# Kernel optimization log

Measured on AMD Instinct MI355X. Metric: run time of the kernel, lower is better.

## Reference

```python
import jax, jax.numpy as jnp
import numpy as np

B, N, F, Tf, Tm, Df, Dm = 8, 128, 128, 64, 256, 32, 128
E, H, TE = 64, 128, 64  # node_emb_dim, hidden_dim, time_emb_dim


def setup_inputs() -> dict:
    key = jax.random.key(0)
    ks = jax.random.split(key, 16)
    s = 0.05
    return {
        'noisy_adj': jax.random.normal(ks[0], (B, N, N), jnp.float32),
        'node_feats': jax.random.normal(ks[1], (B, N, F), jnp.float32),
        'feat_fnirs': jax.random.normal(ks[2], (B, N, Tf, Df), jnp.float32),
        'feat_music': jax.random.normal(ks[3], (B, 1, Tm, Dm), jnp.float32),
        'g_pre': jax.random.normal(ks[4], (B, N, N), jnp.float32),
        'node_W': jax.random.normal(ks[5], (F, E), jnp.float32) * s,
        'node_b': jnp.zeros((E,), jnp.float32),
        'fnirs_W': jax.random.normal(ks[6], (Df, H), jnp.float32) * s,
        'fnirs_b': jnp.zeros((H,), jnp.float32),
        'music_W': jax.random.normal(ks[7], (Dm, H), jnp.float32) * s,
        'music_b': jnp.zeros((H,), jnp.float32),
        'mlp_W1': jax.random.normal(ks[8], (2 * E + 2 + H + TE, H), jnp.float32) * s,
        'mlp_b1': jnp.zeros((H,), jnp.float32),
        'mlp_W2': jax.random.normal(ks[9], (H, 1), jnp.float32) * s,
        'mlp_b2': jnp.zeros((1,), jnp.float32),
        't': jax.random.randint(ks[10], (B,), 0, Tf),
    }


def _time_embedding(t_idx):
    # sinusoidal timestep embedding -> [B, TE]
    half = TE // 2
    inv_freq = jnp.exp(-jnp.arange(half, dtype=jnp.float32) * (jnp.log(10000.0) / (half - 1)))
    freqs = t_idx.astype(jnp.float32)[:, None] * inv_freq  # [B, half]
    return jnp.concatenate([jnp.sin(freqs), jnp.cos(freqs)], axis=-1)


def _conditional(feat_fnirs, feat_music, fnirs_W, fnirs_b, music_W, music_b):
    # cross-attention: fNIRS timesteps attend over music timesteps
    q = feat_fnirs @ fnirs_W + fnirs_b          # [B,N,Tf,H]
    kv = feat_music @ music_W + music_b         # [B,1,Tm,H]
    scale = 1.0 / jnp.sqrt(jnp.float32(H))
    scores = jnp.einsum('bnfh,bomh->bnfm', q, kv) * scale  # [B,N,Tf,Tm]
    attn = jax.nn.softmax(scores, axis=-1)
    ctx = jnp.einsum('bnfm,bomh->bnfh', attn, kv)
    fused = q + ctx                              # [B,N,Tf,H]
    attn_weights = attn.mean(axis=1)             # mean across channels -> [B,Tf,Tm]
    ent = -(attn * jnp.log(attn + 1e-8)).sum(-1)
    attention_loss = ent.mean()
    return fused, attn_weights, attention_loss


def reference(noisy_adj, node_feats, feat_fnirs, feat_music, g_pre,
              node_W, node_b, fnirs_W, fnirs_b, music_W, music_b,
              mlp_W1, mlp_b1, mlp_W2, mlp_b2, t):
    h = node_feats @ node_W + node_b             # [B,N,E]

    fused, attn_weights, attention_loss = _conditional(
        feat_fnirs, feat_music, fnirs_W, fnirs_b, music_W, music_b)

    t_idx = jnp.clip(t, 0, fused.shape[2] - 1)
    # gather conditional state at diffusion step t -> [B,N,H]
    idx = jnp.broadcast_to(t_idx[:, None, None, None], (B, N, 1, H))
    cond_t = jnp.take_along_axis(fused, idx, axis=2)[:, :, 0, :]

    time_emb = _time_embedding(t_idx)            # [B,TE]

    # Fused edge MLP layer-1: split W1 along the concat axis instead of
    # materializing the [B,N,N,in_dim] concat tensor (same math).
    W1_hi = mlp_W1[:E]
    W1_hj = mlp_W1[E:2 * E]
    w_adj = mlp_W1[2 * E]          # [H]
    w_gpre = mlp_W1[2 * E + 1]     # [H]
    W1_cond = mlp_W1[2 * E + 2:2 * E + 2 + H]
    W1_time = mlp_W1[2 * E + 2 + H:]

    pre = ((h @ W1_hi)[:, :, None, :]            # h_i varies over row i
           + (h @ W1_hj)[:, None, :, :]          # h_j varies over col j
           + noisy_adj[..., None] * w_adj
           + g_pre[..., None] * w_gpre
           + (cond_t @ W1_cond)[:, None, :, :]   # cond broadcast over row i
           + (time_emb @ W1_time)[:, None, None, :]
           + mlp_b1)                             # [B,N,N,H]
    hid = jax.nn.relu(pre)
    noise_pred = (hid @ mlp_W2)[..., 0] + mlp_b2[0]  # [B,N,N]
    return noise_pred, attn_weights, attention_loss
```

## Files before the change

kernel.cpp:

```cpp
#include <hip/hip_runtime.h>
#include <hip/hip_bf16.h>

#define Bn  8
#define Nn  128
#define Fn  128
#define Tfn 64
#define Tmn 256
#define Dfn 32
#define Dmn 128
#define En  64
#define Hn  128
#define TEn 64

#define OUT_AW_OFF   (Bn*Nn*Nn)
#define OUT_LOSS_OFF (Bn*Nn*Nn + Bn*Tfn*Tmn)

#define WS_G     0
#define WS_BIAS  32768
#define WS_KVT   34816
#define WS_FWT   165888
#define WS_NWT   167936
#define WS_HIT   172032
#define WS_HJT   176128
#define WS_CONDT 180224
#define WS_TVEC  188416
#define WS_PI    189440
#define WS_PJ    320512
#define WS_LOSS  451584

#define SCALE 0.08838834764831845f

typedef __attribute__((ext_vector_type(8))) short short8;
typedef __attribute__((ext_vector_type(4))) float f32x4;

__device__ __forceinline__ unsigned short f2bf(float x) {
  __hip_bfloat16 h = __float2bfloat16(x);
  return __builtin_bit_cast(unsigned short, h);
}
__device__ __forceinline__ unsigned int pk2(float a, float b) {
  return (unsigned int)f2bf(a) | ((unsigned int)f2bf(b) << 16);
}

__global__ __launch_bounds__(128) void k_prep(
    const float* __restrict__ feat_music, const float* __restrict__ music_W,
    const float* __restrict__ music_b, const float* __restrict__ fnirs_W,
    const float* __restrict__ fnirs_b,
    const float* __restrict__ W1, const float* __restrict__ b1,
    const float* __restrict__ node_W, const int* __restrict__ t,
    unsigned short* __restrict__ kvT, unsigned short* __restrict__ G_bf,
    float* __restrict__ bias,
    unsigned short* __restrict__ fwt, unsigned short* __restrict__ nwt,
    unsigned short* __restrict__ hit, unsigned short* __restrict__ hjt,
    unsigned short* __restrict__ condt, float* __restrict__ tvec,
    float* __restrict__ loss_acc)
{
  __shared__ float fm_s[Dmn];
  __shared__ float kv_s[Hn];
  __shared__ float red[2];
  __shared__ float te_l[TEn];
  int tid = threadIdx.x;

  if (blockIdx.x < 2048) {
    int b = blockIdx.x >> 8;
    int m = blockIdx.x & 255;
    fm_s[tid] = feat_music[((size_t)b*Tmn + m)*Dmn + tid];
    __syncthreads();
    float a = music_b[tid];
    #pragma unroll 8
    for (int d = 0; d < Dmn; d++) a = fmaf(fm_s[d], music_W[d*Hn + tid], a);
    kv_s[tid] = a;
    kvT[((size_t)b*Hn + tid)*Tmn + m] = f2bf(a);
    float bp = fnirs_b[tid] * a;
    bp += __shfl_xor(bp, 32); bp += __shfl_xor(bp, 16); bp += __shfl_xor(bp, 8);
    bp += __shfl_xor(bp, 4);  bp += __shfl_xor(bp, 2);  bp += __shfl_xor(bp, 1);
    if ((tid & 63) == 0) red[tid >> 6] = bp;
    __syncthreads();
    int d = tid >> 2, qd = tid & 3;
    float g = 0.f;
    #pragma unroll 8
    for (int hh = 0; hh < 32; hh++) {
      int h = hh*4 + qd;
      g = fmaf(fnirs_W[d*Hn + h], kv_s[h], g);
    }
    g += __shfl_xor(g, 1); g += __shfl_xor(g, 2);
    if (qd == 0) G_bf[((size_t)b*Tmn + m)*Dfn + d] = f2bf(g * SCALE);
    if (tid == 0) bias[b*Tmn + m] = (red[0] + red[1]) * SCALE;
    return;
  }

  int blk = blockIdx.x - 2048;
  if (blk < 8) {
    int b = blk;
    if (tid < TEn/2) {
      int tcl = min(max(t[b], 0), Tfn - 1);
      float fr = (float)tcl * __expf(-(float)tid * (logf(10000.f) / (TEn/2 - 1)));
      te_l[tid] = __sinf(fr);
      te_l[tid + TEn/2] = __cosf(fr);
    }
    __syncthreads();
    float a = b1[tid];
    #pragma unroll 8
    for (int u = 0; u < TEn; u++) a = fmaf(te_l[u], W1[(2*En + 2 + Hn + u)*Hn + tid], a);
    tvec[b*Hn + tid] = a;
    if (b == 0 && tid == 0) loss_acc[0] = 0.f;
  } else if (blk < 16) {
    int q = blk - 8;
    #pragma unroll 4
    for (int i = 0; i < 16; i++) {
      int k = q*16 + i;
      condt[k*Hn + tid] = f2bf(W1[(2*En + 2 + tid)*Hn + k]);
    }
  } else if (blk < 20) {
    int q = blk - 16;
    int e = tid & 63, kh = tid >> 6;
    #pragma unroll 4
    for (int i = 0; i < 16; i++) {
      int k = q*32 + kh*16 + i;
      hit[k*En + e] = f2bf(W1[e*Hn + k]);
    }
  } else if (blk < 24) {
    int q = blk - 20;
    int e = tid & 63, kh = tid >> 6;
    #pragma unroll 4
    for (int i = 0; i < 16; i++) {
      int k = q*32 + kh*16 + i;
      hjt[k*En + e] = f2bf(W1[(En + e)*Hn + k]);
    }
  } else if (blk < 32) {
    int q = blk - 24;
    int fl = tid & 15, eh = tid >> 4;
    #pragma unroll 4
    for (int i = 0; i < 8; i++) {
      int e = eh*8 + i;
      nwt[e*Fn + q*16 + fl] = f2bf(node_W[(q*16 + fl)*En + e]);
    }
  } else if (blk < 34) {
    int q = blk - 32;
    int d = tid & 31, hh = tid >> 5;
    #pragma unroll 4
    for (int i = 0; i < 16; i++) {
      int h = q*64 + hh*16 + i;
      fwt[h*Dfn + d] = f2bf(fnirs_W[d*Hn + h]);
    }
  }
}

struct SmemAttn {
  unsigned short feat_l[Nn][40];
  unsigned short G_l[Tmn][40];
  float bias_l[Tmn];
  float aw_l[4][Tmn];
  float ent_l[4];
};
struct SmemCond {
  unsigned short featT_l[16][40];
  unsigned short A_l[16][264];
  unsigned short nf_l[16][136];
  unsigned short h_l[16][72];
  unsigned short cond_l[16][136];
  float sS[4][16];
  float tvec_l[Hn];
};
union __align__(16) SmemK2 {
  SmemAttn a;
  SmemCond c;
};

__global__ __launch_bounds__(256, 2) void k_attn_cond(
    const float* __restrict__ feat_fnirs, const float* __restrict__ node_feats,
    const float* __restrict__ node_b, const int* __restrict__ t,
    const unsigned short* __restrict__ G_bf, const float* __restrict__ bias,
    const unsigned short* __restrict__ kvT, const unsigned short* __restrict__ fwt,
    const unsigned short* __restrict__ nwt, const unsigned short* __restrict__ hit,
    const unsigned short* __restrict__ hjt, const unsigned short* __restrict__ condt,
    const float* __restrict__ tvec, float* __restrict__ Pi, float* __restrict__ Pj,
    float* __restrict__ aw_out, float* __restrict__ loss_acc)
{
  __shared__ SmemK2 smem;
  int tid = threadIdx.x;
  int lane = tid & 63, wv = tid >> 6;
  int col = lane & 15, kq = lane >> 4;

  if (blockIdx.x < 512) {
    int b = blockIdx.x >> 6, f = blockIdx.x & 63;
    {
      const uint4* gg = (const uint4*)(G_bf + (size_t)b*Tmn*Dfn);
      #pragma unroll
      for (int v0 = 0; v0 < 4; v0++) {
        int v = tid + v0*256;
        uint4 x = gg[v];
        int m = v >> 2, qt = v & 3;
        *((uint4*)&smem.a.G_l[m][qt*8]) = x;
      }
      smem.a.bias_l[tid] = bias[b*Tmn + tid];
      int n = tid >> 1, hf = tid & 1;
      const float* src = feat_fnirs + (((size_t)b*Nn + n)*Tfn + f)*Dfn + hf*16;
      float4 x0 = ((const float4*)src)[0];
      float4 x1 = ((const float4*)src)[1];
      float4 x2 = ((const float4*)src)[2];
      float4 x3 = ((const float4*)src)[3];
      uint4 pa, pb;
      pa.x = pk2(x0.x, x0.y); pa.y = pk2(x0.z, x0.w);
      pa.z = pk2(x1.x, x1.y); pa.w = pk2(x1.z, x1.w);
      pb.x = pk2(x2.x, x2.y); pb.y = pk2(x2.z, x2.w);
      pb.z = pk2(x3.x, x3.y); pb.w = pk2(x3.z, x3.w);
      uint4* dst = (uint4*)&smem.a.feat_l[n][hf*16];
      dst[0] = pa; dst[1] = pb;
    }
    __syncthreads();

    int n0 = wv * 32;
    short8 a0 = *(const short8*)&smem.a.feat_l[n0 + col][kq*8];
    short8 a1 = *(const short8*)&smem.a.feat_l[n0 + 16 + col][kq*8];

    float S0[4] = {0,0,0,0}, S1[4] = {0,0,0,0};
    float T0[4] = {0,0,0,0}, T1[4] = {0,0,0,0};
    float p0[16][4], p1[16][4];

    #pragma unroll
    for (int mt = 0; mt < 16; mt++) {
      short8 bfr = *(const short8*)&smem.a.G_l[mt*16 + col][kq*8];
      float bv = smem.a.bias_l[mt*16 + col];
      f32x4 c0 = __builtin_amdgcn_mfma_f32_16x16x32_bf16(a0, bfr, (f32x4){0.f,0.f,0.f,0.f}, 0, 0, 0);
      f32x4 c1 = __builtin_amdgcn_mfma_f32_16x16x32_bf16(a1, bfr, (f32x4){0.f,0.f,0.f,0.f}, 0, 0, 0);
      #pragma unroll
      for (int r = 0; r < 4; r++) {
        float sc = c0[r] + bv;
        float p = __expf(sc);
        S0[r] += p; T0[r] = fmaf(p, sc, T0[r]); p0[mt][r] = p;
        sc = c1[r] + bv;
        p = __expf(sc);
        S1[r] += p; T1[r] = fmaf(p, sc, T1[r]); p1[mt][r] = p;
      }
    }

    #pragma unroll
    for (int r = 0; r < 4; r++) {
      #pragma unroll
      for (int off = 1; off < 16; off <<= 1) {
        S0[r] += __shfl_xor(S0[r], off);
        S1[r] += __shfl_xor(S1[r], off);
        T0[r] += __shfl_xor(T0[r], off);
        T1[r] += __shfl_xor(T1[r], off);
      }
    }
    float i0v[4], i1v[4];
    #pragma unroll
    for (int r = 0; r < 4; r++) { i0v[r] = 1.f / S0[r]; i1v[r] = 1.f / S1[r]; }

    float ent = 0.f;
    if (col == 0) {
      #pragma unroll
      for (int r = 0; r < 4; r++) {
        ent += (__logf(S0[r]) - T0[r] * i0v[r]);
        ent += (__logf(S1[r]) - T1[r] * i1v[r]);
      }
    }
    ent += __shfl_xor(ent, 32); ent += __shfl_xor(ent, 16);
    ent += __shfl_xor(ent, 8);  ent += __shfl_xor(ent, 4);
    ent += __shfl_xor(ent, 2);  ent += __shfl_xor(ent, 1);
    if (lane == 0) smem.a.ent_l[wv] = ent;

    #pragma unroll
    for (int mt = 0; mt < 16; mt++) {
      float a = 0.f;
      #pragma unroll
      for (int r = 0; r < 4; r++) {
        a = fmaf(p0[mt][r], i0v[r], a);
        a = fmaf(p1[mt][r], i1v[r], a);
      }
      a += __shfl_xor(a, 16);
      a += __shfl_xor(a, 32);
      if (lane < 16) smem.a.aw_l[wv][mt*16 + lane] = a;
    }
    __syncthreads();

    float s = (smem.a.aw_l[0][tid] + smem.a.aw_l[1][tid]) +
              (smem.a.aw_l[2][tid] + smem.a.aw_l[3][tid]);
    aw_out[((size_t)b*Tfn + f)*Tmn + tid] = s * (1.f/(float)Nn);
    if (tid == 0)
      atomicAdd(loss_acc, (smem.a.ent_l[0] + smem.a.ent_l[1]) +
                          (smem.a.ent_l[2] + smem.a.ent_l[3]));
    return;
  }

  int blk = blockIdx.x - 512;
  int b = blk >> 3;
  int i0 = (blk & 7) << 4;
  int tcl = min(max(t[b], 0), Tfn - 1);

  if (tid < 128) {
    int i = tid >> 3, c = (tid & 7) * 4;
    const float* src = feat_fnirs + (((size_t)b*Nn + i0 + i)*Tfn + tcl)*Dfn + c;
    float4 x = *(const float4*)src;
    *(unsigned int*)&smem.c.featT_l[i][c]     = pk2(x.x, x.y);
    *(unsigned int*)&smem.c.featT_l[i][c + 2] = pk2(x.z, x.w);
    smem.c.tvec_l[tid] = tvec[b*Hn + tid];
  }
  {
    int i = tid >> 4, c = (tid & 15) * 8;
    const float* src = node_feats + ((size_t)b*Nn + i0 + i)*Fn + c;
    float4 x0 = ((const float4*)src)[0];
    float4 x1 = ((const float4*)src)[1];
    *(unsigned int*)&smem.c.nf_l[i][c]     = pk2(x0.x, x0.y);
    *(unsigned int*)&smem.c.nf_l[i][c + 2] = pk2(x0.z, x0.w);
    *(unsigned int*)&smem.c.nf_l[i][c + 4] = pk2(x1.x, x1.y);
    *(unsigned int*)&smem.c.nf_l[i][c + 6] = pk2(x1.z, x1.w);
  }
  __syncthreads();

  short8 a_feat = *(const short8*)&smem.c.featT_l[col][kq*8];

  float p[4][4];
  float Sp[4] = {0,0,0,0};
  #pragma unroll
  for (int mtl = 0; mtl < 4; mtl++) {
    int mt = wv*4 + mtl;
    short8 bg = *(const short8*)(G_bf + ((size_t)b*Tmn + mt*16 + col)*Dfn + kq*8);
    f32x4 c = __builtin_amdgcn_mfma_f32_16x16x32_bf16(a_feat, bg, (f32x4){0.f,0.f,0.f,0.f}, 0, 0, 0);
    float bv = bias[b*Tmn + mt*16 + col];
    #pragma unroll
    for (int r = 0; r < 4; r++) {
      float pp = __expf(c[r] + bv);
      p[mtl][r] = pp;
      Sp[r] += pp;
    }
  }
  #pragma unroll
  for (int r = 0; r < 4; r++) {
    float v = Sp[r];
    v += __shfl_xor(v, 1); v += __shfl_xor(v, 2);
    v += __shfl_xor(v, 4); v += __shfl_xor(v, 8);
    Sp[r] = v;
  }
  if (col == 0) {
    #pragma unroll
    for (int r = 0; r < 4; r++) smem.c.sS[wv][kq*4 + r] = Sp[r];
  }
  __syncthreads();
  float invS[4];
  #pragma unroll
  for (int r = 0; r < 4; r++)
    invS[r] = 1.f / (smem.c.sS[0][kq*4+r] + smem.c.sS[1][kq*4+r] +
                     smem.c.sS[2][kq*4+r] + smem.c.sS[3][kq*4+r]);
  #pragma unroll
  for (int mtl = 0; mtl < 4; mtl++) {
    #pragma unroll
    for (int r = 0; r < 4; r++)
      smem.c.A_l[kq*4 + r][(wv*4 + mtl)*16 + col] = f2bf(p[mtl][r] * invS[r]);
  }
  __syncthreads();

  f32x4 accC0 = {0.f,0.f,0.f,0.f}, accC1 = {0.f,0.f,0.f,0.f};
  {
    int ct0 = wv*2, ct1 = wv*2 + 1;
    short8 bq0 = *(const short8*)(fwt + (size_t)(ct0*16 + col)*Dfn + kq*8);
    short8 bq1 = *(const short8*)(fwt + (size_t)(ct1*16 + col)*Dfn + kq*8);
    accC0 = __builtin_amdgcn_mfma_f32_16x16x32_bf16(a_feat, bq0, accC0, 0, 0, 0);
    accC1 = __builtin_amdgcn_mfma_f32_16x16x32_bf16(a_feat, bq1, accC1, 0, 0, 0);
    #pragma unroll
    for (int ks = 0; ks < 8; ks++) {
      short8 aA = *(const short8*)&smem.c.A_l[col][ks*32 + kq*8];
      short8 bk0 = *(const short8*)(kvT + ((size_t)b*Hn + ct0*16 + col)*Tmn + ks*32 + kq*8);
      short8 bk1 = *(const short8*)(kvT + ((size_t)b*Hn + ct1*16 + col)*Tmn + ks*32 + kq*8);
      accC0 = __builtin_amdgcn_mfma_f32_16x16x32_bf16(aA, bk0, accC0, 0, 0, 0);
      accC1 = __builtin_amdgcn_mfma_f32_16x16x32_bf16(aA, bk1, accC1, 0, 0, 0);
    }
  }
  f32x4 accH = {0.f,0.f,0.f,0.f};
  #pragma unroll
  for (int ks = 0; ks < 4; ks++) {
    short8 aN = *(const short8*)&smem.c.nf_l[col][ks*32 + kq*8];
    short8 bn = *(const short8*)(nwt + (size_t)(wv*16 + col)*Fn + ks*32 + kq*8);
    accH = __builtin_amdgcn_mfma_f32_16x16x32_bf16(aN, bn, accH, 0, 0, 0);
  }
  float nb = node_b[wv*16 + col];
  #pragma unroll
  for (int r = 0; r < 4; r++) {
    smem.c.cond_l[kq*4 + r][(wv*2    )*16 + col] = f2bf(accC0[r]);
    smem.c.cond_l[kq*4 + r][(wv*2 + 1)*16 + col] = f2bf(accC1[r]);
    smem.c.h_l[kq*4 + r][wv*16 + col] = f2bf(accH[r] + nb);
  }
  __syncthreads();

  short8 aH[2];
  aH[0] = *(const short8*)&smem.c.h_l[col][kq*8];
  aH[1] = *(const short8*)&smem.c.h_l[col][32 + kq*8];
  #pragma unroll
  for (int ctl = 0; ctl < 2; ctl++) {
    int ct = wv*2 + ctl;
    f32x4 accPi = {0.f,0.f,0.f,0.f}, accPj = {0.f,0.f,0.f,0.f};
    #pragma unroll
    for (int ks = 0; ks < 2; ks++) {
      short8 bi_ = *(const short8*)(hit + (size_t)(ct*16 + col)*En + ks*32 + kq*8);
      short8 bj_ = *(const short8*)(hjt + (size_t)(ct*16 + col)*En + ks*32 + kq*8);
      accPi = __builtin_amdgcn_mfma_f32_16x16x32_bf16(aH[ks], bi_, accPi, 0, 0, 0);
      accPj = __builtin_amdgcn_mfma_f32_16x16x32_bf16(aH[ks], bj_, accPj, 0, 0, 0);
    }
    #pragma unroll
    for (int ks = 0; ks < 4; ks++) {
      short8 aC = *(const short8*)&smem.c.cond_l[col][ks*32 + kq*8];
      short8 bc = *(const short8*)(condt + (size_t)(ct*16 + col)*Hn + ks*32 + kq*8);
      accPj = __builtin_amdgcn_mfma_f32_16x16x32_bf16(aC, bc, accPj, 0, 0, 0);
    }
    float tv = smem.c.tvec_l[ct*16 + col];
    #pragma unroll
    for (int r = 0; r < 4; r++) {
      size_t row = (size_t)b*Nn + i0 + kq*4 + r;
      Pi[row*Hn + ct*16 + col] = accPi[r];
      Pj[row*Hn + ct*16 + col] = accPj[r] + tv;
    }
  }
}

__global__ __launch_bounds__(256) void k_edge(
    const float* __restrict__ adj, const float* __restrict__ gpre,
    const float* __restrict__ W1, const float* __restrict__ W2,
    const float* __restrict__ b2p, const float* __restrict__ Pi,
    const float* __restrict__ Pj, float* __restrict__ out,
    const float* __restrict__ loss_acc)
{
  int b  = blockIdx.x >> 6;
  int ib = (blockIdx.x >> 1) & 31;
  int jh = blockIdx.x & 1;
  int i0 = ib * 4;
  int tid = threadIdx.x;

  __shared__ float4 Pj_s4[64*32];
  __shared__ float4 Pi_s4[4*32];
  __shared__ float4 w2_s[32], wa_s[32], wg_s[32];

  {
    const float4* Pjg = (const float4*)(Pj + ((size_t)b*Nn + jh*64)*Hn);
    #pragma unroll
    for (int v0 = 0; v0 < 8; v0++) {
      int idx = tid + v0*256;
      int j = idx >> 5, c = idx & 31;
      Pj_s4[j*32 + (c ^ (j & 31))] = Pjg[j*32 + c];
    }
    if (tid < 128) {
      int r = tid >> 5, c = tid & 31;
      Pi_s4[r*32 + c] = ((const float4*)(Pi + ((size_t)b*Nn + i0 + r)*Hn))[c];
    } else if (tid < 160) {
      int c = tid - 128;
      w2_s[c] = ((const float4*)W2)[c];
      wa_s[c] = ((const float4*)(W1 + (2*En)*Hn))[c];
      wg_s[c] = ((const float4*)(W1 + (2*En + 1)*Hn))[c];
    }
  }
  __syncthreads();

  int r = tid >> 6, lane = tid & 63;
  int i = i0 + r, j = jh*64 + lane;
  float b2v = b2p[0];
  float adjv = adj [((size_t)b*Nn + i)*Nn + j];
  float gpv  = gpre[((size_t)b*Nn + i)*Nn + j];
  float a0 = 0.f, a1 = 0.f, a2 = 0.f, a3 = 0.f;
  #pragma unroll
  for (int c = 0; c < 32; c++) {
    float4 pj = Pj_s4[lane*32 + (c ^ (lane & 31))];
    float4 pi = Pi_s4[r*32 + c];
    float4 wa = wa_s[c], wg = wg_s[c], w2 = w2_s[c];
    float e0 = pi.x + pj.x + adjv*wa.x + gpv*wg.x;
    float e1 = pi.y + pj.y + adjv*wa.y + gpv*wg.y;
    float e2 = pi.z + pj.z + adjv*wa.z + gpv*wg.z;
    float e3 = pi.w + pj.w + adjv*wa.w + gpv*wg.w;
    a0 = fmaf(fmaxf(e0, 0.f), w2.x, a0);
    a1 = fmaf(fmaxf(e1, 0.f), w2.y, a1);
    a2 = fmaf(fmaxf(e2, 0.f), w2.z, a2);
    a3 = fmaf(fmaxf(e3, 0.f), w2.w, a3);
  }
  out[((size_t)b*Nn + i)*Nn + j] = (a0 + a1) + (a2 + a3) + b2v;

  if (blockIdx.x == 0 && tid == 0)
    out[OUT_LOSS_OFF] = loss_acc[0] * (1.f / (float)(Bn*Nn*Tfn));
}

extern "C" void kernel_launch(void* const* d_in, const int* in_sizes, int n_in,
                              void* d_out, int out_size, void* d_ws, size_t ws_size,
                              hipStream_t stream) {
  (void)in_sizes; (void)n_in; (void)out_size; (void)ws_size;
  const float* noisy_adj  = (const float*)d_in[0];
  const float* node_feats = (const float*)d_in[1];
  const float* feat_fnirs = (const float*)d_in[2];
  const float* feat_music = (const float*)d_in[3];
  const float* g_pre      = (const float*)d_in[4];
  const float* node_W     = (const float*)d_in[5];
  const float* node_b     = (const float*)d_in[6];
  const float* fnirs_W    = (const float*)d_in[7];
  const float* fnirs_b    = (const float*)d_in[8];
  const float* music_W    = (const float*)d_in[9];
  const float* music_b    = (const float*)d_in[10];
  const float* mlp_W1     = (const float*)d_in[11];
  const float* mlp_b1     = (const float*)d_in[12];
  const float* mlp_W2     = (const float*)d_in[13];
  const float* mlp_b2     = (const float*)d_in[14];
  const int*   t          = (const int*)d_in[15];

  float* out = (float*)d_out;
  float* ws = (float*)d_ws;
  unsigned short* g_ws    = (unsigned short*)(ws + WS_G);
  float*          bias_ws = ws + WS_BIAS;
  unsigned short* kvt_ws  = (unsigned short*)(ws + WS_KVT);
  unsigned short* fwt_ws  = (unsigned short*)(ws + WS_FWT);
  unsigned short* nwt_ws  = (unsigned short*)(ws + WS_NWT);
  unsigned short* hit_ws  = (unsigned short*)(ws + WS_HIT);
  unsigned short* hjt_ws  = (unsigned short*)(ws + WS_HJT);
  unsigned short* cndt_ws = (unsigned short*)(ws + WS_CONDT);
  float*          tvec_ws = ws + WS_TVEC;
  float*          Pi_ws   = ws + WS_PI;
  float*          Pj_ws   = ws + WS_PJ;
  float*          loss_ws = ws + WS_LOSS;

  k_prep     <<<2082, 128, 0, stream>>>(feat_music, music_W, music_b, fnirs_W,
                                        fnirs_b, mlp_W1, mlp_b1, node_W, t,
                                        kvt_ws, g_ws, bias_ws, fwt_ws, nwt_ws,
                                        hit_ws, hjt_ws, cndt_ws, tvec_ws, loss_ws);
  k_attn_cond<<<576,  256, 0, stream>>>(feat_fnirs, node_feats, node_b, t,
                                        g_ws, bias_ws, kvt_ws, fwt_ws, nwt_ws,
                                        hit_ws, hjt_ws, cndt_ws, tvec_ws,
                                        Pi_ws, Pj_ws, out + OUT_AW_OFF, loss_ws);
  k_edge     <<<512,  256, 0, stream>>>(noisy_adj, g_pre, mlp_W1, mlp_W2, mlp_b2,
                                        Pi_ws, Pj_ws, out, loss_ws);
}
```

Measured before the change: 131.4 us.

## Split weight prep and compute music KV/G projections with bf16 MFMA tiles

The old prep kernel ran 2048 tiny blocks, each doing a scalar FMA loop for one music timestep's KV projection and its G/bias products. The new version moves the weight transposes into a small 37-block kernel that also packs bf16 music_W and an fnirs_W+bias matrix. It adds a 64-block kernel that computes KV, G and bias for 32 timesteps at a time with 16x16x32 bf16 MFMAs. The goal is to remove scalar FMA work and the launch overhead of many tiny blocks, at the cost of an extra kernel launch and bf16 rounding of feat_music and of KV before the G product.

```diff
diff --git a/kernel.cpp b/kernel.cpp
--- a/kernel.cpp
+++ b/kernel.cpp
@@ -27,6 +27,8 @@
 #define WS_PI    189440
 #define WS_PJ    320512
 #define WS_LOSS  451584
+#define WS_MWT   451588
+#define WS_FWB   459780
 
 #define SCALE 0.08838834764831845f
 
@@ -41,56 +43,21 @@
   return (unsigned int)f2bf(a) | ((unsigned int)f2bf(b) << 16);
 }
 
-__global__ __launch_bounds__(128) void k_prep(
-    const float* __restrict__ feat_music, const float* __restrict__ music_W,
-    const float* __restrict__ music_b, const float* __restrict__ fnirs_W,
-    const float* __restrict__ fnirs_b,
+__global__ __launch_bounds__(128) void k_wprep(
     const float* __restrict__ W1, const float* __restrict__ b1,
-    const float* __restrict__ node_W, const int* __restrict__ t,
-    unsigned short* __restrict__ kvT, unsigned short* __restrict__ G_bf,
-    float* __restrict__ bias,
+    const float* __restrict__ node_W, const float* __restrict__ fnirs_W,
+    const float* __restrict__ fnirs_b, const float* __restrict__ music_W,
+    const int* __restrict__ t,
     unsigned short* __restrict__ fwt, unsigned short* __restrict__ nwt,
     unsigned short* __restrict__ hit, unsigned short* __restrict__ hjt,
-    unsigned short* __restrict__ condt, float* __restrict__ tvec,
+    unsigned short* __restrict__ condt, unsigned short* __restrict__ mwt,
+    unsigned short* __restrict__ fwb, float* __restrict__ tvec,
     float* __restrict__ loss_acc)
 {
-  __shared__ float fm_s[Dmn];
-  __shared__ float kv_s[Hn];
-  __shared__ float red[2];
-  __shared__ float te_l[TEn];
-  int tid = threadIdx.x;
-
-  if (blockIdx.x < 2048) {
-    int b = blockIdx.x >> 8;
-    int m = blockIdx.x & 255;
-    fm_s[tid] = feat_music[((size_t)b*Tmn + m)*Dmn + tid];
-    __syncthreads();
-    float a = music_b[tid];
-    #pragma unroll 8
-    for (int d = 0; d < Dmn; d++) a = fmaf(fm_s[d], music_W[d*Hn + tid], a);
-    kv_s[tid] = a;
-    kvT[((size_t)b*Hn + tid)*Tmn + m] = f2bf(a);
-    float bp = fnirs_b[tid] * a;
-    bp += __shfl_xor(bp, 32); bp += __shfl_xor(bp, 16); bp += __shfl_xor(bp, 8);
-    bp += __shfl_xor(bp, 4);  bp += __shfl_xor(bp, 2);  bp += __shfl_xor(bp, 1);
-    if ((tid & 63) == 0) red[tid >> 6] = bp;
-    __syncthreads();
-    int d = tid >> 2, qd = tid & 3;
-    float g = 0.f;
-    #pragma unroll 8
-    for (int hh = 0; hh < 32; hh++) {
-      int h = hh*4 + qd;
-      g = fmaf(fnirs_W[d*Hn + h], kv_s[h], g);
-    }
-    g += __shfl_xor(g, 1); g += __shfl_xor(g, 2);
-    if (qd == 0) G_bf[((size_t)b*Tmn + m)*Dfn + d] = f2bf(g * SCALE);
-    if (tid == 0) bias[b*Tmn + m] = (red[0] + red[1]) * SCALE;
-    return;
-  }
-
-  int blk = blockIdx.x - 2048;
+  int blk = blockIdx.x, tid = threadIdx.x;
   if (blk < 8) {
     int b = blk;
+    __shared__ float te_l[TEn];
     if (tid < TEn/2) {
       int tcl = min(max(t[b], 0), Tfn - 1);
       float fr = (float)tcl * __expf(-(float)tid * (logf(10000.f) / (TEn/2 - 1)));
@@ -141,6 +108,108 @@
     for (int i = 0; i < 16; i++) {
       int h = q*64 + hh*16 + i;
       fwt[h*Dfn + d] = f2bf(fnirs_W[d*Hn + h]);
+    }
+  } else if (blk < 36) {
+    int q = blk - 34;
+    #pragma unroll 4
+    for (int i = 0; i < 64; i++) {
+      int h = q*64 + i;
+      mwt[h*Dmn + tid] = f2bf(music_W[(size_t)tid*Hn + h]);
+    }
+  } else {
+    #pragma unroll 4
+    for (int row = 0; row < 48; row++) {
+      float v = (row < 32) ? fnirs_W[row*Hn + tid] : (row == 32 ? fnirs_b[tid] : 0.f);
+      fwb[row*Hn + tid] = f2bf(v);
+    }
+  }
+}
+
+__global__ __launch_bounds__(256) void k_music(
+    const float* __restrict__ feat_music, const float* __restrict__ music_b,
+    const unsigned short* __restrict__ mwt, const unsigned short* __restrict__ fwb,
+    unsigned short* __restrict__ kvT, unsigned short* __restrict__ G_bf,
+    float* __restrict__ bias)
+{
+  __shared__ unsigned short fm_l[32][136];
+  __shared__ unsigned short kv_l[32][136];
+
+  int tid = threadIdx.x;
+  int b = blockIdx.x >> 3;
+  int m0 = (blockIdx.x & 7) << 5;
+
+  {
+    int m = tid >> 3, c = (tid & 7) * 16;
+    const float* src = feat_music + ((size_t)b*Tmn + m0 + m)*Dmn + c;
+    float4 x0 = ((const float4*)src)[0];
+    float4 x1 = ((const float4*)src)[1];
+    float4 x2 = ((const float4*)src)[2];
+    float4 x3 = ((const float4*)src)[3];
+    uint4 pa, pb;
+    pa.x = pk2(x0.x, x0.y); pa.y = pk2(x0.z, x0.w);
+    pa.z = pk2(x1.x, x1.y); pa.w = pk2(x1.z, x1.w);
+    pb.x = pk2(x2.x, x2.y); pb.y = pk2(x2.z, x2.w);
+    pb.z = pk2(x3.x, x3.y); pb.w = pk2(x3.z, x3.w);
+    uint4* dst = (uint4*)&fm_l[m][c];
+    dst[0] = pa; dst[1] = pb;
+  }
+  __syncthreads();
+
+  int lane = tid & 63, wv = tid >> 6;
+  int col = lane & 15, kq = lane >> 4;
+  int rt = wv & 1, cp = wv >> 1;
+
+  short8 aF[4];
+  #pragma unroll
+  for (int ks = 0; ks < 4; ks++)
+    aF[ks] = *(const short8*)&fm_l[rt*16 + col][ks*32 + kq*8];
+
+  #pragma unroll
+  for (int htl = 0; htl < 4; htl++) {
+    int ht = cp*4 + htl;
+    int h = ht*16 + col;
+    f32x4 acc = {0.f,0.f,0.f,0.f};
+    #pragma unroll
+    for (int ks = 0; ks < 4; ks++) {
+      short8 bfr = *(const short8*)(mwt + (size_t)h*Dmn + ks*32 + kq*8);
+      acc = __builtin_amdgcn_mfma_f32_16x16x32_bf16(aF[ks], bfr, acc, 0, 0, 0);
+    }
+    float mb = music_b[h];
+    unsigned short kvb[4];
+    #pragma unroll
+    for (int r = 0; r < 4; r++) {
+      float v = acc[r] + mb;
+      kvb[r] = f2bf(v);
+      kv_l[rt*16 + kq*4 + r][h] = kvb[r];
+    }
+    *(ushort4*)(kvT + ((size_t)b*Hn + h)*Tmn + m0 + rt*16 + kq*4) =
+        make_ushort4(kvb[0], kvb[1], kvb[2], kvb[3]);
+  }
+  __syncthreads();
+
+  short8 aK[4];
+  #pragma unroll
+  for (int ks = 0; ks < 4; ks++)
+    aK[ks] = *(const short8*)&kv_l[rt*16 + col][ks*32 + kq*8];
+
+  int nct = (cp == 0) ? 2 : 1;
+  for (int cti = 0; cti < nct; cti++) {
+    int ct = (cp == 0) ? cti*2 : 1;
+    f32x4 acc = {0.f,0.f,0.f,0.f};
+    #pragma unroll
+    for (int ks = 0; ks < 4; ks++) {
+      short8 bfr = *(const short8*)(fwb + (size_t)(ct*16 + col)*Hn + ks*32 + kq*8);
+      acc = __builtin_amdgcn_mfma_f32_16x16x32_bf16(aK[ks], bfr, acc, 0, 0, 0);
+    }
+    if (ct < 2) {
+      #pragma unroll
+      for (int r = 0; r < 4; r++)
+        G_bf[((size_t)b*Tmn + m0 + rt*16 + kq*4 + r)*Dfn + ct*16 + col] =
+            f2bf(acc[r] * SCALE);
+    } else if (col == 0) {
+      #pragma unroll
+      for (int r = 0; r < 4; r++)
+        bias[(size_t)b*Tmn + m0 + rt*16 + kq*4 + r] = acc[r] * SCALE;
     }
   }
 }
@@ -511,11 +580,14 @@
   float*          Pi_ws   = ws + WS_PI;
   float*          Pj_ws   = ws + WS_PJ;
   float*          loss_ws = ws + WS_LOSS;
-
-  k_prep     <<<2082, 128, 0, stream>>>(feat_music, music_W, music_b, fnirs_W,
-                                        fnirs_b, mlp_W1, mlp_b1, node_W, t,
-                                        kvt_ws, g_ws, bias_ws, fwt_ws, nwt_ws,
-                                        hit_ws, hjt_ws, cndt_ws, tvec_ws, loss_ws);
+  unsigned short* mwt_ws  = (unsigned short*)(ws + WS_MWT);
+  unsigned short* fwb_ws  = (unsigned short*)(ws + WS_FWB);
+
+  k_wprep    <<<37,   128, 0, stream>>>(mlp_W1, mlp_b1, node_W, fnirs_W, fnirs_b,
+                                        music_W, t, fwt_ws, nwt_ws, hit_ws, hjt_ws,
+                                        cndt_ws, mwt_ws, fwb_ws, tvec_ws, loss_ws);
+  k_music    <<<64,   256, 0, stream>>>(feat_music, music_b, mwt_ws, fwb_ws,
+                                        kvt_ws, g_ws, bias_ws);
   k_attn_cond<<<576,  256, 0, stream>>>(feat_fnirs, node_feats, node_b, t,
                                         g_ws, bias_ws, kvt_ws, fwt_ws, nwt_ws,
                                         hit_ws, hjt_ws, cndt_ws, tvec_ws,
```

Result: slower. 136.5 us (+3.9%).
